# Optimization experiments

Measured on AMD Instinct MI355X. Metric: run time of the kernel, lower is better.

## Reference

```python
import jax, jax.numpy as jnp
import numpy as np

BOX_SIZE = 256
POS_ENC_DIM = 10


def positional_encoding_geom2(coords, enc_dim, DD):
    # coords: [..., 3] -> [..., 3*enc_dim*2]
    D2 = DD // 2
    i = jnp.arange(enc_dim, dtype=coords.dtype)
    freqs = D2 * (1.0 / D2) ** (i / (enc_dim - 1))  # [enc_dim]
    k = coords[..., None] * freqs  # [..., 3, enc_dim]
    x = jnp.concatenate([jnp.sin(k), jnp.cos(k)], axis=-1)  # [..., 3, 2*enc_dim]
    return x.reshape(*x.shape[:-2], -1)


def setup_inputs() -> dict:
    key = jax.random.key(0)
    ks = jax.random.split(key, 6)
    B, N, L, H, n_layers = 8, 50000, 32, 128, 6
    in_dim = 3 * POS_ENC_DIM * 2 + L  # 92
    return {
        "z0": jax.random.normal(ks[0], (B, L), dtype=jnp.float32),
        "cons": jax.random.uniform(ks[1], (N, 3), dtype=jnp.float32),
        "w_lin0": jax.random.normal(ks[2], (H, in_dim), dtype=jnp.float32) * (in_dim ** -0.5),
        "w_deform": jax.random.normal(ks[3], (n_layers, H, H), dtype=jnp.float32) * (H ** -0.5),
        "w_lin1a": jax.random.normal(ks[4], (3, H), dtype=jnp.float32) * (H ** -0.5),
        "w_lin1b": jax.random.normal(ks[5], (3, 3), dtype=jnp.float32) * 0.1,
    }


def reference(z0, cons, w_lin0, w_deform, w_lin1a, w_lin1b):
    B = z0.shape[0]
    N = cons.shape[0]
    # positional encoding of consensus points: [N, 60]
    cons_pos = positional_encoding_geom2(cons, POS_ENC_DIM, BOX_SIZE)
    posi = jnp.broadcast_to(cons, (B, N, 3))
    posi_n = jnp.broadcast_to(cons_pos, (B, N, cons_pos.shape[-1]))
    conf_feat = jnp.broadcast_to(z0[:, None, :], (B, N, z0.shape[-1]))
    x = jnp.concatenate([posi_n, conf_feat], axis=2)  # [B, N, 92]
    # lin0 (bias-free) -> deform stack of ELU(Linear) blocks
    x = jnp.einsum('bnf,of->bno', x, w_lin0)  # [B, N, H]
    for j in range(w_deform.shape[0]):
        x = jax.nn.elu(jnp.einsum('bnh,oh->bno', x, w_deform[j]))
    res = jax.nn.elu(jnp.einsum('bnh,oh->bno', x, w_lin1a))  # [B, N, 3]
    res = jnp.einsum('bni,oi->bno', res, w_lin1b)  # [B, N, 3]
    pos = posi + res
    resn = res
    return (pos, resn)
```

## Files before the change

### kernel.cpp

```cpp
#include <hip/hip_runtime.h>
#include <hip/hip_bf16.h>
#include <math.h>

typedef _Float16 half8 __attribute__((ext_vector_type(8)));
typedef float    f32x4 __attribute__((ext_vector_type(4)));

#define NPTS  50000
#define BATCH 8

__device__ __forceinline__ void gload_lds16(const void* g, void* l) {
    __builtin_amdgcn_global_load_lds(
        (const __attribute__((address_space(1))) unsigned int*)g,
        (__attribute__((address_space(3))) unsigned int*)l, 16, 0, 0);
}

__global__ void prep_weights_k(const float* __restrict__ w_lin0,
                               const float* __restrict__ w_def,
                               const float* __restrict__ w1a,
                               _Float16* __restrict__ W)
{
    int idx = blockIdx.x * blockDim.x + threadIdx.x;
    if (idx >= 8*128*128) return;
    int slot = idx >> 14;
    int o    = (idx >> 7) & 127;
    int pos  = idx & 127;
    int ks = pos >> 5, l = pos & 31, gg = l >> 3, jj = l & 7;
    int k = ks*32 + 16*(jj>>2) + 4*gg + (jj&3);
    float v = 0.f;
    if (slot == 0) {
        if (k < 60)                 v = w_lin0[o*92 + k];
        else if (k >= 64 && k < 96) v = w_lin0[o*92 + 60 + (k-64)];
    } else if (slot <= 6) {
        v = w_def[(slot-1)*16384 + o*128 + k];
    } else {
        if (o < 3) v = w1a[o*128 + k];
    }
    int pos_sw = pos ^ ((o & 7) << 3);
    W[slot*16384 + o*128 + pos_sw] = (_Float16)v;
}

__global__ __launch_bounds__(256, 2)
void decoder_main(const float* __restrict__ z0,
                  const float* __restrict__ cons,
                  const _Float16* __restrict__ W,
                  const float* __restrict__ w1b,
                  float* __restrict__ out)
{
    __shared__ __align__(16) unsigned char smem[65536];
    float* res_f = (float*)smem;

    const int t    = threadIdx.x;
    const int lane = t & 63;
    const int wid  = t >> 6;
    const int p    = lane & 15;
    const int g    = lane >> 4;
    const int n0   = blockIdx.x * 32;

    auto stage = [&](int slot, int buf) {
        const unsigned char* src = (const unsigned char*)(W + slot*16384) + t*16;
        unsigned char* dst = smem + buf*32768 + t*16;
        #pragma unroll
        for (int i = 0; i < 8; ++i)
            gload_lds16(src + i*4096, dst + i*4096);
    };

    stage(0, 0);

    half8 Bw[4][4];
    #pragma unroll
    for (int pt = 0; pt < 4; ++pt) {
        int lrow = wid*64 + pt*16 + p;
        int n = n0 + (lrow >> 3); if (n >= NPTS) n = NPTS - 1;
        int b = lrow & 7;
        float c0 = cons[n*3+0], c1 = cons[n*3+1], c2 = cons[n*3+2];
        #pragma unroll
        for (int ks = 0; ks < 2; ++ks) {
            half8 h;
            #pragma unroll
            for (int j = 0; j < 8; ++j) {
                int k = ks*32 + 16*(j>>2) + 4*g + (j&3);
                float v = 0.f;
                if (k < 60) {
                    int c = k/20, rem = k%20, i = rem%10;
                    float f  = exp2f(7.f * (1.f - (float)i * (1.f/9.f)));
                    float cc = (c == 0) ? c0 : (c == 1) ? c1 : c2;
                    float a  = cc * f;
                    v = (rem < 10) ? __sinf(a) : __cosf(a);
                }
                h[j] = (_Float16)v;
            }
            Bw[pt][ks] = h;
        }
        {
            half8 h;
            #pragma unroll
            for (int j = 0; j < 8; ++j) {
                int zi = 16*(j>>2) + 4*g + (j&3);
                h[j] = (_Float16)z0[b*32 + zi];
            }
            Bw[pt][2] = h;
        }
        {
            half8 h;
            #pragma unroll
            for (int j = 0; j < 8; ++j) h[j] = (_Float16)0.f;
            Bw[pt][3] = h;
        }
    }

    __syncthreads();
    stage(1, 1);

    for (int j = 0; j < 7; ++j) {
        const unsigned char* wb = smem + (j & 1)*32768;
        f32x4 acc[4][8];
        #pragma unroll
        for (int pt = 0; pt < 4; ++pt)
            #pragma unroll
            for (int ft = 0; ft < 8; ++ft)
                acc[pt][ft] = f32x4{0.f, 0.f, 0.f, 0.f};

        #pragma unroll
        for (int ft = 0; ft < 8; ++ft) {
            int row = ft*16 + p;
            int sw  = (row & 7) << 4;
            half8 A[4];
            #pragma unroll
            for (int ks = 0; ks < 4; ++ks)
                A[ks] = *(const half8*)(wb + row*256 + ((ks*64 + g*16) ^ sw));
            #pragma unroll
            for (int ks = 0; ks < 4; ++ks)
                #pragma unroll
                for (int pt = 0; pt < 4; ++pt)
                    acc[pt][ft] = __builtin_amdgcn_mfma_f32_16x16x32_f16(
                        A[ks], Bw[pt][ks], acc[pt][ft], 0, 0, 0);
        }

        __syncthreads();
        if (j <= 5) stage(j + 2, j & 1);

        #pragma unroll
        for (int pt = 0; pt < 4; ++pt) {
            #pragma unroll
            for (int ks = 0; ks < 4; ++ks) {
                half8 h;
                #pragma unroll
                for (int e = 0; e < 4; ++e) {
                    float v = acc[pt][2*ks][e];
                    v = (j == 0 || v > 0.f) ? v : (__expf(v) - 1.f);
                    h[e] = (_Float16)v;
                }
                #pragma unroll
                for (int e = 0; e < 4; ++e) {
                    float v = acc[pt][2*ks+1][e];
                    v = (j == 0 || v > 0.f) ? v : (__expf(v) - 1.f);
                    h[4+e] = (_Float16)v;
                }
                Bw[pt][ks] = h;
            }
        }
    }

    {
        const unsigned char* wb = smem + 32768;
        f32x4 a1[4];
        #pragma unroll
        for (int pt = 0; pt < 4; ++pt) a1[pt] = f32x4{0.f, 0.f, 0.f, 0.f};
        int row = p;
        int sw  = (row & 7) << 4;
        half8 A[4];
        #pragma unroll
        for (int ks = 0; ks < 4; ++ks)
            A[ks] = *(const half8*)(wb + row*256 + ((ks*64 + g*16) ^ sw));
        #pragma unroll
        for (int ks = 0; ks < 4; ++ks)
            #pragma unroll
            for (int pt = 0; pt < 4; ++pt)
                a1[pt] = __builtin_amdgcn_mfma_f32_16x16x32_f16(
                    A[ks], Bw[pt][ks], a1[pt], 0, 0, 0);

        if (g == 0) {
            #pragma unroll
            for (int pt = 0; pt < 4; ++pt) {
                int lrow = wid*64 + pt*16 + p;
                #pragma unroll
                for (int e = 0; e < 3; ++e) {
                    float v = a1[pt][e];
                    v = (v > 0.f) ? v : (__expf(v) - 1.f);
                    res_f[lrow*3 + e] = v;
                }
            }
        }
    }
    __syncthreads();

    for (int idx = t; idx < 1536; idx += 256) {
        int arr = idx >> 9 >= 1 ? (idx >= 768) : 0;
        arr = idx / 768;
        int e  = idx % 768;
        int b  = e / 96;
        int q  = e % 96;
        int nl = q / 3;
        int i  = q % 3;
        int rowl = nl*8 + b;
        float r0 = res_f[rowl*3+0], r1 = res_f[rowl*3+1], r2 = res_f[rowl*3+2];
        float rv = w1b[i*3+0]*r0 + w1b[i*3+1]*r1 + w1b[i*3+2]*r2;
        int n = n0 + nl;
        if (n < NPTS) {
            if (arr) out[BATCH*NPTS*3 + (b*NPTS + n)*3 + i] = rv;
            else     out[(b*NPTS + n)*3 + i] = cons[n*3+i] + rv;
        }
    }
}

extern "C" void kernel_launch(void* const* d_in, const int* in_sizes, int n_in,
                              void* d_out, int out_size, void* d_ws, size_t ws_size,
                              hipStream_t stream)
{
    const float* z0     = (const float*)d_in[0];
    const float* cons   = (const float*)d_in[1];
    const float* w_lin0 = (const float*)d_in[2];
    const float* w_def  = (const float*)d_in[3];
    const float* w1a    = (const float*)d_in[4];
    const float* w1b    = (const float*)d_in[5];
    _Float16* W = (_Float16*)d_ws;

    prep_weights_k<<<(8*128*128 + 255)/256, 256, 0, stream>>>(w_lin0, w_def, w1a, W);
    int nblk = (NPTS + 31) / 32;
    decoder_main<<<nblk, 256, 0, stream>>>(z0, cons, W, w1b, (float*)d_out);
}
```

Baseline: 200.9 us.

## Drop LDS weight staging; stream MFMA weights directly from global per wave

Replaces the 256-thread block that double-buffered weight slabs into LDS with single-wave blocks of 8 points, each loading its A-operand fragments straight from global memory (L2-cached) with a register double-buffer across output tiles. This removes the block-wide barriers and the 64KB LDS footprint, so more waves can be resident. It also skips the unused K chunk in layer 0 and writes outputs directly from registers without an LDS round trip. The cost is that every wave re-reads the full weight set from cache, which raises L2/L1 traffic and exposes global load latency.

```diff
diff --git a/kernel.cpp b/kernel.cpp
--- a/kernel.cpp
+++ b/kernel.cpp
@@ -7,12 +7,6 @@
 
 #define NPTS  50000
 #define BATCH 8
-
-__device__ __forceinline__ void gload_lds16(const void* g, void* l) {
-    __builtin_amdgcn_global_load_lds(
-        (const __attribute__((address_space(1))) unsigned int*)g,
-        (__attribute__((address_space(3))) unsigned int*)l, 16, 0, 0);
-}
 
 __global__ void prep_weights_k(const float* __restrict__ w_lin0,
                                const float* __restrict__ w_def,
@@ -35,43 +29,29 @@
     } else {
         if (o < 3) v = w1a[o*128 + k];
     }
-    int pos_sw = pos ^ ((o & 7) << 3);
-    W[slot*16384 + o*128 + pos_sw] = (_Float16)v;
+    W[idx] = (_Float16)v;
 }
 
-__global__ __launch_bounds__(256, 2)
+__global__ __launch_bounds__(64, 2)
 void decoder_main(const float* __restrict__ z0,
                   const float* __restrict__ cons,
                   const _Float16* __restrict__ W,
                   const float* __restrict__ w1b,
                   float* __restrict__ out)
 {
-    __shared__ __align__(16) unsigned char smem[65536];
-    float* res_f = (float*)smem;
-
-    const int t    = threadIdx.x;
-    const int lane = t & 63;
-    const int wid  = t >> 6;
-    const int p    = lane & 15;
-    const int g    = lane >> 4;
-    const int n0   = blockIdx.x * 32;
-
-    auto stage = [&](int slot, int buf) {
-        const unsigned char* src = (const unsigned char*)(W + slot*16384) + t*16;
-        unsigned char* dst = smem + buf*32768 + t*16;
-        #pragma unroll
-        for (int i = 0; i < 8; ++i)
-            gload_lds16(src + i*4096, dst + i*4096);
-    };
-
-    stage(0, 0);
+    const int lane = threadIdx.x;
+    const int p = lane & 15;
+    const int g = lane >> 4;
+    const int n0 = blockIdx.x * 8;
+
+    const f32x4 Z = {0.f, 0.f, 0.f, 0.f};
 
     half8 Bw[4][4];
     #pragma unroll
     for (int pt = 0; pt < 4; ++pt) {
-        int lrow = wid*64 + pt*16 + p;
-        int n = n0 + (lrow >> 3); if (n >= NPTS) n = NPTS - 1;
-        int b = lrow & 7;
+        const int lrow = pt*16 + p;
+        const int n = n0 + (lrow >> 3);
+        const int b = lrow & 7;
         float c0 = cons[n*3+0], c1 = cons[n*3+1], c2 = cons[n*3+2];
         #pragma unroll
         for (int ks = 0; ks < 2; ++ks) {
@@ -91,124 +71,139 @@
             }
             Bw[pt][ks] = h;
         }
-        {
-            half8 h;
-            #pragma unroll
-            for (int j = 0; j < 8; ++j) {
-                int zi = 16*(j>>2) + 4*g + (j&3);
-                h[j] = (_Float16)z0[b*32 + zi];
-            }
-            Bw[pt][2] = h;
-        }
-        {
-            half8 h;
-            #pragma unroll
-            for (int j = 0; j < 8; ++j) h[j] = (_Float16)0.f;
-            Bw[pt][3] = h;
-        }
-    }
-
-    __syncthreads();
-    stage(1, 1);
-
-    for (int j = 0; j < 7; ++j) {
-        const unsigned char* wb = smem + (j & 1)*32768;
-        f32x4 acc[4][8];
+        half8 hz;
+        #pragma unroll
+        for (int j = 0; j < 8; ++j)
+            hz[j] = (_Float16)z0[b*32 + 16*(j>>2) + 4*g + (j&3)];
+        Bw[pt][2] = hz;
+        #pragma unroll
+        for (int j = 0; j < 8; ++j) Bw[pt][3][j] = (_Float16)0.f;
+    }
+
+    f32x4 acc[4][8];
+
+    {
+        const unsigned char* a0 = (const unsigned char*)W + p*256 + g*16;
+        half8 A[2][3];
+        #pragma unroll
+        for (int ks = 0; ks < 3; ++ks) A[0][ks] = *(const half8*)(a0 + ks*64);
+        #pragma unroll
+        for (int ft = 0; ft < 8; ++ft) {
+            if (ft < 7) {
+                const unsigned char* an = a0 + (ft+1)*4096;
+                #pragma unroll
+                for (int ks = 0; ks < 3; ++ks) A[(ft+1)&1][ks] = *(const half8*)(an + ks*64);
+            }
+            #pragma unroll
+            for (int pt = 0; pt < 4; ++pt)
+                acc[pt][ft] = __builtin_amdgcn_mfma_f32_16x16x32_f16(A[ft&1][0], Bw[pt][0], Z, 0, 0, 0);
+            #pragma unroll
+            for (int ks = 1; ks < 3; ++ks)
+                #pragma unroll
+                for (int pt = 0; pt < 4; ++pt)
+                    acc[pt][ft] = __builtin_amdgcn_mfma_f32_16x16x32_f16(A[ft&1][ks], Bw[pt][ks], acc[pt][ft], 0, 0, 0);
+        }
+    }
+
+    for (int j = 1; j <= 6; ++j) {
+        const unsigned char* a0 = (const unsigned char*)W + j*32768 + p*256 + g*16;
+        half8 A[2][4];
+        #pragma unroll
+        for (int ks = 0; ks < 4; ++ks) A[0][ks] = *(const half8*)(a0 + ks*64);
+
         #pragma unroll
         for (int pt = 0; pt < 4; ++pt)
-            #pragma unroll
-            for (int ft = 0; ft < 8; ++ft)
-                acc[pt][ft] = f32x4{0.f, 0.f, 0.f, 0.f};
-
-        #pragma unroll
-        for (int ft = 0; ft < 8; ++ft) {
-            int row = ft*16 + p;
-            int sw  = (row & 7) << 4;
-            half8 A[4];
-            #pragma unroll
-            for (int ks = 0; ks < 4; ++ks)
-                A[ks] = *(const half8*)(wb + row*256 + ((ks*64 + g*16) ^ sw));
-            #pragma unroll
-            for (int ks = 0; ks < 4; ++ks)
-                #pragma unroll
-                for (int pt = 0; pt < 4; ++pt)
-                    acc[pt][ft] = __builtin_amdgcn_mfma_f32_16x16x32_f16(
-                        A[ks], Bw[pt][ks], acc[pt][ft], 0, 0, 0);
-        }
-
-        __syncthreads();
-        if (j <= 5) stage(j + 2, j & 1);
-
-        #pragma unroll
-        for (int pt = 0; pt < 4; ++pt) {
             #pragma unroll
             for (int ks = 0; ks < 4; ++ks) {
                 half8 h;
                 #pragma unroll
                 for (int e = 0; e < 4; ++e) {
-                    float v = acc[pt][2*ks][e];
-                    v = (j == 0 || v > 0.f) ? v : (__expf(v) - 1.f);
-                    h[e] = (_Float16)v;
-                }
-                #pragma unroll
-                for (int e = 0; e < 4; ++e) {
-                    float v = acc[pt][2*ks+1][e];
-                    v = (j == 0 || v > 0.f) ? v : (__expf(v) - 1.f);
-                    h[4+e] = (_Float16)v;
+                    float v0 = acc[pt][2*ks][e];
+                    float v1 = acc[pt][2*ks+1][e];
+                    if (j >= 2) {
+                        v0 = (v0 > 0.f) ? v0 : (__expf(v0) - 1.f);
+                        v1 = (v1 > 0.f) ? v1 : (__expf(v1) - 1.f);
+                    }
+                    h[e]   = (_Float16)v0;
+                    h[4+e] = (_Float16)v1;
                 }
                 Bw[pt][ks] = h;
             }
-        }
-    }
-
+
+        #pragma unroll
+        for (int ft = 0; ft < 8; ++ft) {
+            if (ft < 7) {
+                const unsigned char* an = a0 + (ft+1)*4096;
+                #pragma unroll
+                for (int ks = 0; ks < 4; ++ks) A[(ft+1)&1][ks] = *(const half8*)(an + ks*64);
+            }
+            #pragma unroll
+            for (int pt = 0; pt < 4; ++pt)
+                acc[pt][ft] = __builtin_amdgcn_mfma_f32_16x16x32_f16(A[ft&1][0], Bw[pt][0], Z, 0, 0, 0);
+            #pragma unroll
+            for (int ks = 1; ks < 4; ++ks)
+                #pragma unroll
+                for (int pt = 0; pt < 4; ++pt)
+                    acc[pt][ft] = __builtin_amdgcn_mfma_f32_16x16x32_f16(A[ft&1][ks], Bw[pt][ks], acc[pt][ft], 0, 0, 0);
+        }
+    }
+
+    #pragma unroll
+    for (int pt = 0; pt < 4; ++pt)
+        #pragma unroll
+        for (int ks = 0; ks < 4; ++ks) {
+            half8 h;
+            #pragma unroll
+            for (int e = 0; e < 4; ++e) {
+                float v0 = acc[pt][2*ks][e];
+                float v1 = acc[pt][2*ks+1][e];
+                v0 = (v0 > 0.f) ? v0 : (__expf(v0) - 1.f);
+                v1 = (v1 > 0.f) ? v1 : (__expf(v1) - 1.f);
+                h[e]   = (_Float16)v0;
+                h[4+e] = (_Float16)v1;
+            }
+            Bw[pt][ks] = h;
+        }
+
+    f32x4 a1[4];
     {
-        const unsigned char* wb = smem + 32768;
-        f32x4 a1[4];
-        #pragma unroll
-        for (int pt = 0; pt < 4; ++pt) a1[pt] = f32x4{0.f, 0.f, 0.f, 0.f};
-        int row = p;
-        int sw  = (row & 7) << 4;
+        const unsigned char* a0 = (const unsigned char*)W + 7*32768 + p*256 + g*16;
         half8 A[4];
         #pragma unroll
-        for (int ks = 0; ks < 4; ++ks)
-            A[ks] = *(const half8*)(wb + row*256 + ((ks*64 + g*16) ^ sw));
-        #pragma unroll
-        for (int ks = 0; ks < 4; ++ks)
+        for (int ks = 0; ks < 4; ++ks) A[ks] = *(const half8*)(a0 + ks*64);
+        #pragma unroll
+        for (int pt = 0; pt < 4; ++pt)
+            a1[pt] = __builtin_amdgcn_mfma_f32_16x16x32_f16(A[0], Bw[pt][0], Z, 0, 0, 0);
+        #pragma unroll
+        for (int ks = 1; ks < 4; ++ks)
             #pragma unroll
             for (int pt = 0; pt < 4; ++pt)
-                a1[pt] = __builtin_amdgcn_mfma_f32_16x16x32_f16(
-                    A[ks], Bw[pt][ks], a1[pt], 0, 0, 0);
-
-        if (g == 0) {
-            #pragma unroll
-            for (int pt = 0; pt < 4; ++pt) {
-                int lrow = wid*64 + pt*16 + p;
-                #pragma unroll
-                for (int e = 0; e < 3; ++e) {
-                    float v = a1[pt][e];
-                    v = (v > 0.f) ? v : (__expf(v) - 1.f);
-                    res_f[lrow*3 + e] = v;
-                }
-            }
-        }
-    }
-    __syncthreads();
-
-    for (int idx = t; idx < 1536; idx += 256) {
-        int arr = idx >> 9 >= 1 ? (idx >= 768) : 0;
-        arr = idx / 768;
-        int e  = idx % 768;
-        int b  = e / 96;
-        int q  = e % 96;
-        int nl = q / 3;
-        int i  = q % 3;
-        int rowl = nl*8 + b;
-        float r0 = res_f[rowl*3+0], r1 = res_f[rowl*3+1], r2 = res_f[rowl*3+2];
-        float rv = w1b[i*3+0]*r0 + w1b[i*3+1]*r1 + w1b[i*3+2]*r2;
-        int n = n0 + nl;
-        if (n < NPTS) {
-            if (arr) out[BATCH*NPTS*3 + (b*NPTS + n)*3 + i] = rv;
-            else     out[(b*NPTS + n)*3 + i] = cons[n*3+i] + rv;
+                a1[pt] = __builtin_amdgcn_mfma_f32_16x16x32_f16(A[ks], Bw[pt][ks], a1[pt], 0, 0, 0);
+    }
+
+    if (g == 0) {
+        float b00=w1b[0],b01=w1b[1],b02=w1b[2];
+        float b10=w1b[3],b11=w1b[4],b12=w1b[5];
+        float b20=w1b[6],b21=w1b[7],b22=w1b[8];
+        #pragma unroll
+        for (int pt = 0; pt < 4; ++pt) {
+            float r0 = a1[pt][0], r1 = a1[pt][1], r2 = a1[pt][2];
+            r0 = (r0 > 0.f) ? r0 : (__expf(r0) - 1.f);
+            r1 = (r1 > 0.f) ? r1 : (__expf(r1) - 1.f);
+            r2 = (r2 > 0.f) ? r2 : (__expf(r2) - 1.f);
+            int row = pt*16 + p;
+            int n = n0 + (row >> 3);
+            int b = row & 7;
+            int obase = (b*NPTS + n)*3;
+            float rv0 = b00*r0 + b01*r1 + b02*r2;
+            float rv1 = b10*r0 + b11*r1 + b12*r2;
+            float rv2 = b20*r0 + b21*r1 + b22*r2;
+            out[obase+0] = cons[n*3+0] + rv0;
+            out[obase+1] = cons[n*3+1] + rv1;
+            out[obase+2] = cons[n*3+2] + rv2;
+            out[BATCH*NPTS*3 + obase+0] = rv0;
+            out[BATCH*NPTS*3 + obase+1] = rv1;
+            out[BATCH*NPTS*3 + obase+2] = rv2;
         }
     }
 }
@@ -225,7 +220,6 @@
     const float* w1b    = (const float*)d_in[5];
     _Float16* W = (_Float16*)d_ws;
 
-    prep_weights_k<<<(8*128*128 + 255)/256, 256, 0, stream>>>(w_lin0, w_def, w1a, W);
-    int nblk = (NPTS + 31) / 32;
-    decoder_main<<<nblk, 256, 0, stream>>>(z0, cons, W, w1b, (float*)d_out);
+    prep_weights_k<<<512, 256, 0, stream>>>(w_lin0, w_def, w1a, W);
+    decoder_main<<<NPTS/8, 64, 0, stream>>>(z0, cons, W, w1b, (float*)d_out);
 }
```

New measurement: 259.9 us. 1.29x slower.
